# Optimization experiments

Measured on AMD Instinct MI355X. Metric: run time of the kernel, lower is better.

Reference implementation:

```python
import jax, jax.numpy as jnp
import numpy as np

V, C, TCTX, H, L = 32000, 768, 1024, 12, 6
B, T = 2, 1024
D = C // H
EPS = 1e-5


def setup_inputs() -> dict:
    key = jax.random.key(0)
    ks = jax.random.split(key, 12)
    s = lambda k, shape: jax.random.normal(k, shape, jnp.float32) * 0.02
    return {
        "x_indices": jax.random.randint(ks[0], (B, T), 0, V, jnp.int32),
        "tok_emb": s(ks[1], (V, C)),
        "pos_emb": s(ks[2], (TCTX, C)),
        "ln1_g": jnp.ones((L, C)), "ln1_b": jnp.zeros((L, C)),
        "wq": s(ks[3], (L, C, C)), "wk": s(ks[4], (L, C, C)), "wv": s(ks[5], (L, C, C)),
        "wo": s(ks[6], (L, C, C)), "bo": jnp.zeros((L, C)),
        "ln2_g": jnp.ones((L, C)), "ln2_b": jnp.zeros((L, C)),
        "w1": s(ks[7], (L, C, 4 * C)), "b1": jnp.zeros((L, 4 * C)),
        "w2": s(ks[8], (L, 4 * C, C)), "b2": jnp.zeros((L, C)),
        "lnf_g": jnp.ones((C,)), "lnf_b": jnp.zeros((C,)),
        "wp": s(ks[9], (C, V)), "bp": jnp.zeros((V,)),
    }


def _ln(x, g, b):
    m = x.mean(-1, keepdims=True)
    v = ((x - m) ** 2).mean(-1, keepdims=True)
    return (x - m) * jax.lax.rsqrt(v + EPS) * g + b


def _forward(x_indices, tok_emb, pos_emb, ln1_g, ln1_b, wq, wk, wv, wo, bo,
             ln2_g, ln2_b, w1, b1, w2, b2, lnf_g, lnf_b, wp, bp):
    Bv, Tv = x_indices.shape
    x = tok_emb[x_indices] + pos_emb[:Tv]  # [B,T,C]
    mask = jnp.tril(jnp.ones((Tv, Tv), dtype=bool))  # causal

    def block(x, p):
        g1, be1, q_w, k_w, v_w, o_w, o_b, g2, be2, f1, fb1, f2, fb2 = p
        h = _ln(x, g1, be1)
        q = (h @ q_w).reshape(Bv, Tv, H, D)
        k = (h @ k_w).reshape(Bv, Tv, H, D)
        v = (h @ v_w).reshape(Bv, Tv, H, D)
        scores = jnp.einsum('bthd,bshd->bhts', q, k) / jnp.sqrt(jnp.float32(D))
        scores = jnp.where(mask, scores, -jnp.inf)
        a = jax.nn.softmax(scores, axis=-1)
        o = jnp.einsum('bhts,bshd->bthd', a, v).reshape(Bv, Tv, C)
        x = x + o @ o_w + o_b
        h2 = _ln(x, g2, be2)
        x = x + jax.nn.relu(h2 @ f1 + fb1) @ f2 + fb2
        return x, None

    layer_params = (ln1_g, ln1_b, wq, wk, wv, wo, bo, ln2_g, ln2_b, w1, b1, w2, b2)
    x, _ = jax.lax.scan(block, x, layer_params)
    x = _ln(x, lnf_g, lnf_b)
    return x @ wp + bp  # logits [B,T,V]


def reference(x_indices, tok_emb, pos_emb, ln1_g, ln1_b, wq, wk, wv, wo, bo,
              ln2_g, ln2_b, w1, b1, w2, b2, lnf_g, lnf_b, wp, bp):
    return _forward(x_indices, tok_emb, pos_emb, ln1_g, ln1_b, wq, wk, wv, wo, bo,
                    ln2_g, ln2_b, w1, b1, w2, b2, lnf_g, lnf_b, wp, bp)
```

## Files before the change

### kernel.cpp

```cpp
#include <hip/hip_runtime.h>
#include <stdint.h>

#define DEV __device__ __forceinline__

typedef unsigned short u16;
typedef __attribute__((ext_vector_type(8))) short short8;
typedef __attribute__((ext_vector_type(4))) float floatx4;

#define B_ 2
#define T_ 1024
#define C_ 768
#define H_ 12
#define L_ 6
#define V_ 32000
#define F_ 3072
#define M_ 2048
#define C3_ 2304

#define VMW(n) asm volatile("s_waitcnt vmcnt(" #n ")" ::: "memory")
#define LGKM0 asm volatile("s_waitcnt lgkmcnt(0)" ::: "memory")
#define SBAR __builtin_amdgcn_s_barrier()
#define SCHED0 __builtin_amdgcn_sched_barrier(0)

DEV u16 f2bf(float f) {
  unsigned int u; __builtin_memcpy(&u, &f, 4);
  u += 0x7FFFu + ((u >> 16) & 1u);
  return (u16)(u >> 16);
}

DEV void gload16(const void* g, void* l) {
  __builtin_amdgcn_global_load_lds(
      (__attribute__((address_space(1))) void*)(uintptr_t)g,
      (__attribute__((address_space(3))) void*)(unsigned int)(uintptr_t)l,
      16, 0, 0);
}

DEV int xcd_swz(int flat, int nwg) {
  int q = nwg >> 3, r = nwg & 7;
  int xcd = flat & 7, sid = flat >> 3;
  return (xcd < r ? xcd * (q + 1) : r * (q + 1) + (xcd - r) * q) + sid;
}

__global__ __launch_bounds__(256) void transpose_f32_bf16(
    const float* __restrict__ src, u16* __restrict__ dst, int R, int Cc,
    size_t src_z, size_t dst_z) {
  __shared__ float tile[32][33];
  const float* s = src + (size_t)blockIdx.z * src_z;
  u16* d = dst + (size_t)blockIdx.z * dst_z;
  int c0 = blockIdx.x * 32, r0 = blockIdx.y * 32;
  int tx = threadIdx.x & 31, ty = threadIdx.x >> 5;
#pragma unroll
  for (int i = 0; i < 4; i++)
    tile[ty + 8 * i][tx] = s[(size_t)(r0 + ty + 8 * i) * Cc + (c0 + tx)];
  __syncthreads();
#pragma unroll
  for (int i = 0; i < 4; i++)
    d[(size_t)(c0 + ty + 8 * i) * R + (r0 + tx)] = f2bf(tile[tx][ty + 8 * i]);
}

__global__ __launch_bounds__(256) void transpose4_qkvo(
    const float* __restrict__ wq, const float* __restrict__ wk,
    const float* __restrict__ wv, const float* __restrict__ wo,
    u16* __restrict__ wqkvT, u16* __restrict__ woT) {
  __shared__ float tile[32][33];
  int z = blockIdx.z;
  int l = z >> 2, wsel = z & 3;
  size_t CC = (size_t)C_ * C_;
  const float* s = (wsel == 0 ? wq : wsel == 1 ? wk : wsel == 2 ? wv : wo) + (size_t)l * CC;
  u16* d = (wsel < 3) ? (wqkvT + (size_t)l * 3 * CC + (size_t)wsel * CC)
                      : (woT + (size_t)l * CC);
  int c0 = blockIdx.x * 32, r0 = blockIdx.y * 32;
  int tx = threadIdx.x & 31, ty = threadIdx.x >> 5;
#pragma unroll
  for (int i = 0; i < 4; i++)
    tile[ty + 8 * i][tx] = s[(size_t)(r0 + ty + 8 * i) * C_ + (c0 + tx)];
  __syncthreads();
#pragma unroll
  for (int i = 0; i < 4; i++)
    d[(size_t)(c0 + ty + 8 * i) * C_ + (r0 + tx)] = f2bf(tile[tx][ty + 8 * i]);
}

__global__ __launch_bounds__(256) void embed_ln(
    const int* __restrict__ idx, const float* __restrict__ tok,
    const float* __restrict__ pos, const float* __restrict__ g,
    const float* __restrict__ b, float* __restrict__ x, u16* __restrict__ out) {
  int row = blockIdx.x;
  int t = row & (T_ - 1);
  int tk = idx[row];
  const float* tp = tok + (size_t)tk * C_;
  const float* pp = pos + (size_t)t * C_;
  float* xp = x + (size_t)row * C_;
  int tid = threadIdx.x;
  float v0 = tp[tid] + pp[tid];
  float v1 = tp[tid + 256] + pp[tid + 256];
  float v2 = tp[tid + 512] + pp[tid + 512];
  xp[tid] = v0; xp[tid + 256] = v1; xp[tid + 512] = v2;
  float s = v0 + v1 + v2;
  float ss = v0 * v0 + v1 * v1 + v2 * v2;
#pragma unroll
  for (int o = 32; o > 0; o >>= 1) { s += __shfl_down(s, o); ss += __shfl_down(ss, o); }
  __shared__ float red[8];
  int wid = tid >> 6;
  if ((tid & 63) == 0) { red[wid] = s; red[4 + wid] = ss; }
  __syncthreads();
  float tot = red[0] + red[1] + red[2] + red[3];
  float tss = red[4] + red[5] + red[6] + red[7];
  float mean = tot * (1.f / C_);
  float var = tss * (1.f / C_) - mean * mean;
  float rstd = rsqrtf(var + 1e-5f);
  u16* op = out + (size_t)row * C_;
  op[tid]       = f2bf((v0 - mean) * rstd * g[tid]       + b[tid]);
  op[tid + 256] = f2bf((v1 - mean) * rstd * g[tid + 256] + b[tid + 256]);
  op[tid + 512] = f2bf((v2 - mean) * rstd * g[tid + 512] + b[tid + 512]);
}

__global__ __launch_bounds__(256) void ln_kernel(
    const float* __restrict__ x, const float* __restrict__ g,
    const float* __restrict__ b, u16* __restrict__ out) {
  int row = blockIdx.x;
  int tid = threadIdx.x;
  const float* xp = x + (size_t)row * C_;
  float v0 = xp[tid], v1 = xp[tid + 256], v2 = xp[tid + 512];
  float s = v0 + v1 + v2;
  float ss = v0 * v0 + v1 * v1 + v2 * v2;
#pragma unroll
  for (int o = 32; o > 0; o >>= 1) { s += __shfl_down(s, o); ss += __shfl_down(ss, o); }
  __shared__ float red[8];
  int wid = tid >> 6;
  if ((tid & 63) == 0) { red[wid] = s; red[4 + wid] = ss; }
  __syncthreads();
  float tot = red[0] + red[1] + red[2] + red[3];
  float tss = red[4] + red[5] + red[6] + red[7];
  float mean = tot * (1.f / C_);
  float var = tss * (1.f / C_) - mean * mean;
  float rstd = rsqrtf(var + 1e-5f);
  u16* op = out + (size_t)row * C_;
  op[tid]       = f2bf((v0 - mean) * rstd * g[tid]       + b[tid]);
  op[tid + 256] = f2bf((v1 - mean) * rstd * g[tid + 256] + b[tid + 256]);
  op[tid + 512] = f2bf((v2 - mean) * rstd * g[tid + 512] + b[tid + 512]);
}

template <int THREADS, int BM, int BN, int WM, int WN, int BIAS, int RELU, int OUTMODE, int SPLITK>
__global__ __launch_bounds__(THREADS) void gemm3(
    const u16* __restrict__ A, const u16* __restrict__ BT,
    const float* __restrict__ bias,
    u16* __restrict__ ob, float* __restrict__ fout, u16* __restrict__ vt,
    int N, int K) {
  constexpr int ALOADS = (BM * 64) / (THREADS * 16);
  constexpr int BLOADS = (BN * 64) / (THREADS * 16);
  constexpr int LDS_L = ALOADS + BLOADS;
  constexpr int MF = BM / (WM * 16);
  constexpr int NF = BN / (WN * 16);
  __shared__ __align__(16) u16 As[3][BM * 32];
  __shared__ __align__(16) u16 Bs[3][BN * 32];

  int tid = threadIdx.x;
  int lane = tid & 63, w = tid >> 6;
  int wm = w / WN, wn = w % WN;
  int rr = lane & 15, qg = lane >> 4;

  int gx = gridDim.x;
  int nwg = gx * gridDim.y;
  int flat = blockIdx.y * gx + blockIdx.x;
  int wg = xcd_swz(flat, nwg);
  int m0 = (wg % gx) * BM, n0 = (wg / gx) * BN;

  int kz = SPLITK > 1 ? blockIdx.z : 0;
  int Keff = SPLITK > 1 ? (K / SPLITK) : K;
  int kbase = kz * Keff;

  const u16* Aps[ALOADS];
  const u16* Bps[BLOADS];
#pragma unroll
  for (int i = 0; i < ALOADS; i++) {
    int idx = i * THREADS + tid;
    int row = idx >> 2;
    int chunk = (idx & 3) ^ ((row >> 1) & 3);
    Aps[i] = A + (size_t)(m0 + row) * K + chunk * 8 + kbase;
  }
#pragma unroll
  for (int i = 0; i < BLOADS; i++) {
    int idx = i * THREADS + tid;
    int row = idx >> 2;
    int chunk = (idx & 3) ^ ((row >> 1) & 3);
    Bps[i] = BT + (size_t)(n0 + row) * K + chunk * 8 + kbase;
  }

  auto stage = [&](int sl, int kk) {
#pragma unroll
    for (int i = 0; i < ALOADS; i++)
      gload16(Aps[i] + kk, (char*)As + (size_t)sl * BM * 64 + i * THREADS * 16 + w * 1024);
#pragma unroll
    for (int i = 0; i < BLOADS; i++)
      gload16(Bps[i] + kk, (char*)Bs + (size_t)sl * BN * 64 + i * THREADS * 16 + w * 1024);
  };

  floatx4 zero = {0.f, 0.f, 0.f, 0.f};
  floatx4 acc[MF][NF];
#pragma unroll
  for (int i = 0; i < MF; i++)
#pragma unroll
    for (int j = 0; j < NF; j++) acc[i][j] = zero;

  int NT = Keff >> 5;
  stage(0, 0);
  stage(1, 32);
  if constexpr (LDS_L == 2) VMW(2);
  else if constexpr (LDS_L == 3) VMW(3);
  else if constexpr (LDS_L == 4) VMW(4);
  else VMW(6);
  SBAR;
  SCHED0;

  int sqA = (qg ^ ((rr >> 1) & 3)) << 4;

  for (int t = 0; t < NT; ++t) {
    int sl = t % 3;
    if (t + 2 < NT) stage((t + 2) % 3, (t + 2) << 5);
    SCHED0;
    const char* Ab = (const char*)As + (size_t)sl * BM * 64;
    const char* Bb = (const char*)Bs + (size_t)sl * BN * 64;
    short8 af[MF], bf[NF];
#pragma unroll
    for (int i = 0; i < MF; i++)
      af[i] = *(const short8*)(Ab + ((wm * (BM / WM) + i * 16 + rr) << 6) + sqA);
#pragma unroll
    for (int j = 0; j < NF; j++)
      bf[j] = *(const short8*)(Bb + ((wn * (BN / WN) + j * 16 + rr) << 6) + sqA);
    __builtin_amdgcn_s_setprio(1);
#pragma unroll
    for (int i = 0; i < MF; i++)
#pragma unroll
      for (int j = 0; j < NF; j++)
        acc[i][j] = __builtin_amdgcn_mfma_f32_16x16x32_bf16(af[i], bf[j], acc[i][j], 0, 0, 0);
    __builtin_amdgcn_s_setprio(0);
    if (t < NT - 2) {
      if constexpr (LDS_L == 2) VMW(2);
      else if constexpr (LDS_L == 3) VMW(3);
      else if constexpr (LDS_L == 4) VMW(4);
      else VMW(6);
    } else if (t == NT - 2) VMW(0);
    if (t < NT - 1) { SBAR; SCHED0; }
  }

  int cb = n0 + wn * (BN / WN);
  int rb = m0 + wm * (BM / WM);
  bool isv = (OUTMODE == 3) && (n0 >= 1536);
#pragma unroll
  for (int i = 0; i < MF; i++) {
#pragma unroll
    for (int j = 0; j < NF; j++) {
      int col = cb + j * 16 + rr;
      float bv = 0.f;
      if (BIAS && kz == 0) bv = bias[col];
      float vals[4];
#pragma unroll
      for (int r = 0; r < 4; r++) {
        float val = acc[i][j][r] + bv;
        if (RELU) val = fmaxf(val, 0.f);
        vals[r] = val;
      }
      int row0 = rb + i * 16 + qg * 4;
      if (isv) {
        int colv = col - 1536;
        int bb = row0 >> 10, t0 = row0 & (T_ - 1);
        uint2 pk;
        pk.x = (unsigned int)f2bf(vals[0]) | ((unsigned int)f2bf(vals[1]) << 16);
        pk.y = (unsigned int)f2bf(vals[2]) | ((unsigned int)f2bf(vals[3]) << 16);
        *(uint2*)&vt[((size_t)bb * C_ + colv) * T_ + t0] = pk;
      } else {
#pragma unroll
        for (int r = 0; r < 4; r++) {
          size_t o = (size_t)(row0 + r) * N + col;
          if (OUTMODE == 0 || OUTMODE == 3) ob[o] = f2bf(vals[r]);
          else if (OUTMODE == 1) {
            if (SPLITK > 1) atomicAdd(&fout[o], vals[r]);
            else fout[o] += vals[r];
          } else fout[o] = vals[r];
        }
      }
    }
  }
}

__global__ __launch_bounds__(512) void gemm8(
    const u16* __restrict__ A, const u16* __restrict__ BT,
    const float* __restrict__ bias, float* __restrict__ fout, int N, int K) {
  __shared__ __align__(16) u16 As[2][2][128 * 64];
  __shared__ __align__(16) u16 Bs[2][2][128 * 64];
  int tid = threadIdx.x;
  int lane = tid & 63, w = tid >> 6;
  int wr = w >> 2, wc = w & 3;
  int rr = lane & 15, qg = lane >> 4;

  int gx = gridDim.x;
  int nwg = gx * gridDim.y;
  int flat = blockIdx.y * gx + blockIdx.x;
  int wg = xcd_swz(flat, nwg);
  int m0 = (wg % gx) * 256, n0 = (wg / gx) * 256;

  int la = tid >> 3;
  int sa = (((tid & 7) ^ (la & 7)) << 3);
  const u16* Ap0 = A + (size_t)(m0 + la) * K + sa;
  const u16* Ap1 = A + (size_t)(m0 + 128 + la) * K + sa;
  int lb0 = la, lb1 = 64 + la;
  const u16* Bp0 = BT + (size_t)(n0 + (lb0 >> 5) * 64 + (lb0 & 31)) * K + sa;
  const u16* Bp1 = BT + (size_t)(n0 + (lb1 >> 5) * 64 + (lb1 & 31)) * K + sa;

  auto stA = [&](int buf, int mh, int kt) {
    size_t off = (size_t)mh * 64 * K + kt * 64;
    gload16(Ap0 + off, (char*)&As[buf][mh][0] + w * 1024);
    gload16(Ap1 + off, (char*)&As[buf][mh][0] + 8192 + w * 1024);
  };
  auto stB = [&](int buf, int nh, int kt) {
    size_t off = (size_t)nh * 32 * K + kt * 64;
    gload16(Bp0 + off, (char*)&Bs[buf][nh][0] + w * 1024);
    gload16(Bp1 + off, (char*)&Bs[buf][nh][0] + 8192 + w * 1024);
  };
  auto stageOrd = [&](int buf, int h, int kt) {
    if (h == 0) stA(buf, 0, kt);
    else if (h == 1) stB(buf, 0, kt);
    else if (h == 2) stB(buf, 1, kt);
    else stA(buf, 1, kt);
  };

  floatx4 zero = {0.f, 0.f, 0.f, 0.f};
  floatx4 acc[8][4];
#pragma unroll
  for (int i = 0; i < 8; i++)
#pragma unroll
    for (int j = 0; j < 4; j++) acc[i][j] = zero;

  short8 a[2][4], b[2][2];
  int NKT = K >> 6;
  int NIT = NKT >> 1;

  stageOrd(0, 0, 0); stageOrd(0, 1, 0); stageOrd(0, 2, 0); stageOrd(0, 3, 0);
  VMW(4);
  SBAR;
  SCHED0;

  for (int it = 0; it < NIT; ++it) {
    int kt2 = it * 2;
    bool last = (it == NIT - 1);
#pragma unroll
    for (int p = 0; p < 8; ++p) {
      const int d = p >> 2;
      const int q = p & 3;
      const int mh = q >> 1, nh = q & 1;
      const char* Abp = (const char*)&As[d][mh][0];
      const char* Bbp = (const char*)&Bs[d][nh][0];
      if (q == 0 || q == 2) {
#pragma unroll
        for (int kk = 0; kk < 2; kk++)
#pragma unroll
          for (int i = 0; i < 4; i++) {
            int l = wr * 64 + i * 16 + rr;
            a[kk][i] = *(const short8*)(Abp + l * 128 + ((((kk << 2) + qg) ^ (rr & 7)) << 4));
          }
      }
#pragma unroll
      for (int kk = 0; kk < 2; kk++)
#pragma unroll
        for (int j = 0; j < 2; j++) {
          int l = wc * 32 + j * 16 + rr;
          b[kk][j] = *(const short8*)(Bbp + l * 128 + ((((kk << 2) + qg) ^ (rr & 7)) << 4));
        }
      if (p < 4) stageOrd(1, q, kt2 + 1);
      else if (!last) stageOrd(0, q, kt2 + 2);
      SCHED0;
      SBAR;
      LGKM0;
      SCHED0;
      __builtin_amdgcn_s_setprio(1);
#pragma unroll
      for (int kk = 0; kk < 2; kk++)
#pragma unroll
        for (int i = 0; i < 4; i++)
#pragma unroll
          for (int j = 0; j < 2; j++)
            acc[mh * 4 + i][nh * 2 + j] = __builtin_amdgcn_mfma_f32_16x16x32_bf16(
                a[kk][i], b[kk][j], acc[mh * 4 + i][nh * 2 + j], 0, 0, 0);
      __builtin_amdgcn_s_setprio(0);
      if (!last || p < 4) VMW(4);
      else if (p == 4) VMW(2);
      else if (p == 5) VMW(0);
      SBAR;
      SCHED0;
    }
  }

  int rbase = m0 + wr * 128;
  int cbase = n0 + wc * 64;
#pragma unroll
  for (int fi = 0; fi < 8; fi++) {
    int row0 = rbase + (fi >> 2) * 64 + (fi & 3) * 16 + qg * 4;
#pragma unroll
    for (int fj = 0; fj < 4; fj++) {
      int col = cbase + (fj >> 1) * 32 + (fj & 1) * 16 + rr;
      float bv = bias[col];
#pragma unroll
      for (int r = 0; r < 4; r++)
        fout[(size_t)(row0 + r) * N + col] = acc[fi][fj][r] + bv;
    }
  }
}

__global__ __launch_bounds__(256) void attn_kernel(
    const u16* __restrict__ qkv, const u16* __restrict__ vt, u16* __restrict__ o) {
  __shared__ __align__(16) u16 P_s[4][16 * 48];
  __shared__ float mls[3][2][16];
  __shared__ float osm[3][16][64];
  int nwg = gridDim.x;
  int wg = xcd_swz(blockIdx.x, nwg);
  int qt = wg & 63;
  int h = (wg >> 6) % H_;
  int b = wg / (64 * H_);
  int q0 = qt << 4;
  int tid = threadIdx.x;
  int ws = tid >> 6;
  int lane = tid & 63;
  int rr = lane & 15, qg = lane >> 4, kq = qg << 3;

  const u16* qb = qkv + (size_t)(b * T_ + q0 + rr) * C3_ + h * 64;
  short8 qf0 = *(const short8*)(qb + kq);
  short8 qf1 = *(const short8*)(qb + 32 + kq);

  float m_r = -1e30f, l_r = 0.f;
  floatx4 zero = {0.f, 0.f, 0.f, 0.f};
  floatx4 oacc[4];
#pragma unroll
  for (int d = 0; d < 4; d++) oacc[d] = zero;

  const u16* kbase = qkv + (size_t)(b * T_) * C3_ + 768 + h * 64;
  const u16* vbase = vt + (size_t)(b * C_ + h * 64) * T_;

  for (int kt0 = ws * 32; kt0 <= q0 + 15; kt0 += 128) {
    floatx4 s[2];
#pragma unroll
    for (int c = 0; c < 2; c++) {
      const u16* kb = kbase + (size_t)(kt0 + c * 16 + rr) * C3_;
      short8 kf0 = *(const short8*)(kb + kq);
      short8 kf1 = *(const short8*)(kb + 32 + kq);
      floatx4 z = zero;
      z = __builtin_amdgcn_mfma_f32_16x16x32_bf16(kf0, qf0, z, 0, 0, 0);
      z = __builtin_amdgcn_mfma_f32_16x16x32_bf16(kf1, qf1, z, 0, 0, 0);
      s[c] = z;
    }
    int qpos = q0 + rr;
    float p[2][4];
    float mx = -1e30f;
#pragma unroll
    for (int c = 0; c < 2; c++)
#pragma unroll
      for (int r = 0; r < 4; r++) {
        int kpos = kt0 + c * 16 + qg * 4 + r;
        float val = s[c][r] * 0.125f;
        val = (kpos <= qpos) ? val : -1e30f;
        p[c][r] = val;
        mx = fmaxf(mx, val);
      }
    mx = fmaxf(mx, __shfl_xor(mx, 16));
    mx = fmaxf(mx, __shfl_xor(mx, 32));
    float mn = fmaxf(m_r, mx);
    float escL = exp2f((m_r - mn) * 1.44269504f);
    m_r = mn;
    float ps = 0.f;
#pragma unroll
    for (int c = 0; c < 2; c++)
#pragma unroll
      for (int r = 0; r < 4; r++) {
        float pv = exp2f((p[c][r] - mn) * 1.44269504f);
        p[c][r] = pv;
        ps += pv;
      }
    ps += __shfl_xor(ps, 16);
    ps += __shfl_xor(ps, 32);
    l_r = l_r * escL + ps;
#pragma unroll
    for (int c = 0; c < 2; c++) {
      unsigned int u0 = (unsigned int)f2bf(p[c][0]) | ((unsigned int)f2bf(p[c][1]) << 16);
      unsigned int u1 = (unsigned int)f2bf(p[c][2]) | ((unsigned int)f2bf(p[c][3]) << 16);
      uint2 pk; pk.x = u0; pk.y = u1;
      *(uint2*)&P_s[ws][rr * 48 + c * 16 + qg * 4] = pk;
    }
    float er[4];
#pragma unroll
    for (int r = 0; r < 4; r++) er[r] = __shfl(escL, qg * 4 + r);
#pragma unroll
    for (int d = 0; d < 4; d++)
#pragma unroll
      for (int r = 0; r < 4; r++) oacc[d][r] *= er[r];
    short8 pa = *(const short8*)&P_s[ws][rr * 48 + kq];
#pragma unroll
    for (int d = 0; d < 4; d++) {
      short8 vf = *(const short8*)(vbase + (size_t)(d * 16 + rr) * T_ + kt0 + kq);
      oacc[d] = __builtin_amdgcn_mfma_f32_16x16x32_bf16(pa, vf, oacc[d], 0, 0, 0);
    }
  }

  if (ws != 0) {
    if (qg == 0) { mls[ws - 1][0][rr] = m_r; mls[ws - 1][1][rr] = l_r; }
#pragma unroll
    for (int d = 0; d < 4; d++)
#pragma unroll
      for (int r = 0; r < 4; r++)
        osm[ws - 1][qg * 4 + r][d * 16 + rr] = oacc[d][r];
  }
  __syncthreads();
  if (ws == 0) {
#pragma unroll
    for (int s2 = 0; s2 < 3; s2++) {
      float mw = mls[s2][0][rr];
      float lw = mls[s2][1][rr];
      float mn = fmaxf(m_r, mw);
      float e0 = exp2f((m_r - mn) * 1.44269504f);
      float e1 = exp2f((mw - mn) * 1.44269504f);
      m_r = mn;
      l_r = l_r * e0 + lw * e1;
      float er0[4], er1[4];
#pragma unroll
      for (int r = 0; r < 4; r++) {
        er0[r] = __shfl(e0, qg * 4 + r);
        er1[r] = __shfl(e1, qg * 4 + r);
      }
#pragma unroll
      for (int d = 0; d < 4; d++)
#pragma unroll
        for (int r = 0; r < 4; r++)
          oacc[d][r] = oacc[d][r] * er0[r] + osm[s2][qg * 4 + r][d * 16 + rr] * er1[r];
    }
    float lb[4];
#pragma unroll
    for (int r = 0; r < 4; r++) lb[r] = __shfl(l_r, qg * 4 + r);
    u16* obp = o + (size_t)(b * T_ + q0) * C_ + h * 64;
#pragma unroll
    for (int d = 0; d < 4; d++)
#pragma unroll
      for (int r = 0; r < 4; r++) {
        int row = qg * 4 + r;
        obp[(size_t)row * C_ + d * 16 + rr] = f2bf(oacc[d][r] / lb[r]);
      }
  }
}

extern "C" void kernel_launch(void* const* d_in, const int* in_sizes, int n_in,
                              void* d_out, int out_size, void* d_ws, size_t ws_size,
                              hipStream_t stream) {
  (void)in_sizes; (void)n_in; (void)out_size; (void)ws_size;
  const int*   xidx = (const int*)d_in[0];
  const float* tok  = (const float*)d_in[1];
  const float* pos  = (const float*)d_in[2];
  const float* ln1g = (const float*)d_in[3];
  const float* ln1b = (const float*)d_in[4];
  const float* wq   = (const float*)d_in[5];
  const float* wk   = (const float*)d_in[6];
  const float* wv   = (const float*)d_in[7];
  const float* wo   = (const float*)d_in[8];
  const float* bo   = (const float*)d_in[9];
  const float* ln2g = (const float*)d_in[10];
  const float* ln2b = (const float*)d_in[11];
  const float* w1   = (const float*)d_in[12];
  const float* b1   = (const float*)d_in[13];
  const float* w2   = (const float*)d_in[14];
  const float* b2   = (const float*)d_in[15];
  const float* lnfg = (const float*)d_in[16];
  const float* lnfb = (const float*)d_in[17];
  const float* wp   = (const float*)d_in[18];
  const float* bp   = (const float*)d_in[19];

  char* ws = (char*)d_ws;
  size_t off = 0;
  auto alloc = [&](size_t bytes) { char* p = ws + off; off += (bytes + 255) & ~(size_t)255; return p; };
  u16* wqkvT = (u16*)alloc((size_t)L_ * 3 * C_ * C_ * 2);
  u16* woT = (u16*)alloc((size_t)L_ * C_ * C_ * 2);
  u16* w1T = (u16*)alloc((size_t)L_ * C_ * F_ * 2);
  u16* w2T = (u16*)alloc((size_t)L_ * C_ * F_ * 2);
  u16* wpT = (u16*)alloc((size_t)C_ * V_ * 2);
  float* x = (float*)alloc((size_t)M_ * C_ * 4);
  u16* hb   = (u16*)alloc((size_t)M_ * C_ * 2);
  u16* qkvb = (u16*)alloc((size_t)M_ * C3_ * 2);
  u16* vtb  = (u16*)alloc((size_t)M_ * C_ * 2);
  u16* aob  = (u16*)alloc((size_t)M_ * C_ * 2);
  u16* mb   = (u16*)alloc((size_t)M_ * F_ * 2);

  dim3 blk(256);
  size_t CC = (size_t)C_ * C_, CF = (size_t)C_ * F_;
  transpose4_qkvo<<<dim3(C_ / 32, C_ / 32, L_ * 4), blk, 0, stream>>>(
      wq, wk, wv, wo, wqkvT, woT);
  transpose_f32_bf16<<<dim3(F_ / 32, C_ / 32, L_), blk, 0, stream>>>(w1, w1T, C_, F_, CF, CF);
  transpose_f32_bf16<<<dim3(C_ / 32, F_ / 32, L_), blk, 0, stream>>>(w2, w2T, F_, C_, CF, CF);
  transpose_f32_bf16<<<dim3(V_ / 32, C_ / 32, 1), blk, 0, stream>>>(wp, wpT, C_, V_, 0, 0);
  embed_ln<<<M_, blk, 0, stream>>>(xidx, tok, pos, ln1g, ln1b, x, hb);

  for (int l = 0; l < L_; ++l) {
    size_t wOff = (size_t)l * 3 * CC;
    size_t oOff = (size_t)l * CC;
    size_t fOff = (size_t)l * CF;
    if (l > 0)
      ln_kernel<<<M_, blk, 0, stream>>>(x, ln1g + l * C_, ln1b + l * C_, hb);
    gemm3<256, 128, 128, 2, 2, 0, 0, 3, 1><<<dim3(M_ / 128, C3_ / 128), 256, 0, stream>>>(
        hb, wqkvT + wOff, nullptr, qkvb, nullptr, vtb, C3_, C_);
    attn_kernel<<<B_ * H_ * (T_ / 16), dim3(256), 0, stream>>>(qkvb, vtb, aob);
    gemm3<256, 128, 128, 2, 2, 1, 0, 1, 2><<<dim3(M_ / 128, C_ / 128, 2), 256, 0, stream>>>(
        aob, woT + oOff, bo + l * C_, nullptr, x, nullptr, C_, C_);
    ln_kernel<<<M_, blk, 0, stream>>>(x, ln2g + l * C_, ln2b + l * C_, hb);
    gemm3<256, 128, 128, 2, 2, 1, 1, 0, 1><<<dim3(M_ / 128, F_ / 128), 256, 0, stream>>>(
        hb, w1T + fOff, b1 + l * F_, mb, nullptr, nullptr, F_, C_);
    gemm3<256, 128, 128, 2, 2, 1, 0, 1, 2><<<dim3(M_ / 128, C_ / 128, 2), 256, 0, stream>>>(
        mb, w2T + fOff, b2 + l * C_, nullptr, x, nullptr, C_, F_);
  }
  ln_kernel<<<M_, blk, 0, stream>>>(x, lnfg, lnfb, hb);
  gemm8<<<dim3(M_ / 256, V_ / 256), 512, 0, stream>>>(
      hb, wpT, bp, (float*)d_out, V_, C_);
}
```

Measured before the change: 1.026 ms.

## Replace split-K atomic residual adds with partial buffers summed in LayerNorm

The Wo and W2 split-K GEMMs now write their two K-partials to separate fp32 buffers with plain stores instead of atomicAdd into the residual. A new ln_sum kernel adds both partials to the residual, writes the updated residual back, and applies the following LayerNorm. This removes atomic read-modify-write traffic and keeps the LN launch count unchanged. In exchange it adds an extra 12 MB partial buffer and additional fp32 reads in the LN kernel.

```diff
diff --git a/kernel.cpp b/kernel.cpp
--- a/kernel.cpp
+++ b/kernel.cpp
@@ -114,13 +114,19 @@
   op[tid + 512] = f2bf((v2 - mean) * rstd * g[tid + 512] + b[tid + 512]);
 }
 
-__global__ __launch_bounds__(256) void ln_kernel(
-    const float* __restrict__ x, const float* __restrict__ g,
-    const float* __restrict__ b, u16* __restrict__ out) {
+__global__ __launch_bounds__(256) void ln_sum(
+    float* __restrict__ x, const float* __restrict__ p0, const float* __restrict__ p1,
+    const float* __restrict__ g, const float* __restrict__ b, u16* __restrict__ out) {
   int row = blockIdx.x;
   int tid = threadIdx.x;
-  const float* xp = x + (size_t)row * C_;
-  float v0 = xp[tid], v1 = xp[tid + 256], v2 = xp[tid + 512];
+  size_t base = (size_t)row * C_;
+  float* xp = x + base;
+  const float* q0 = p0 + base;
+  const float* q1 = p1 + base;
+  float v0 = xp[tid]       + q0[tid]       + q1[tid];
+  float v1 = xp[tid + 256] + q0[tid + 256] + q1[tid + 256];
+  float v2 = xp[tid + 512] + q0[tid + 512] + q1[tid + 512];
+  xp[tid] = v0; xp[tid + 256] = v1; xp[tid + 512] = v2;
   float s = v0 + v1 + v2;
   float ss = v0 * v0 + v1 * v1 + v2 * v2;
 #pragma unroll
@@ -246,6 +252,8 @@
   int cb = n0 + wn * (BN / WN);
   int rb = m0 + wm * (BM / WM);
   bool isv = (OUTMODE == 3) && (n0 >= 1536);
+  float* fo = fout;
+  if (OUTMODE == 4) fo = fout + (size_t)kz * M_ * N;
 #pragma unroll
   for (int i = 0; i < MF; i++) {
 #pragma unroll
@@ -273,10 +281,7 @@
         for (int r = 0; r < 4; r++) {
           size_t o = (size_t)(row0 + r) * N + col;
           if (OUTMODE == 0 || OUTMODE == 3) ob[o] = f2bf(vals[r]);
-          else if (OUTMODE == 1) {
-            if (SPLITK > 1) atomicAdd(&fout[o], vals[r]);
-            else fout[o] += vals[r];
-          } else fout[o] = vals[r];
+          else fo[o] = vals[r];
         }
       }
     }
@@ -578,11 +583,13 @@
   u16* w2T = (u16*)alloc((size_t)L_ * C_ * F_ * 2);
   u16* wpT = (u16*)alloc((size_t)C_ * V_ * 2);
   float* x = (float*)alloc((size_t)M_ * C_ * 4);
+  float* ps0 = (float*)alloc((size_t)2 * M_ * C_ * 4);
   u16* hb   = (u16*)alloc((size_t)M_ * C_ * 2);
   u16* qkvb = (u16*)alloc((size_t)M_ * C3_ * 2);
   u16* vtb  = (u16*)alloc((size_t)M_ * C_ * 2);
   u16* aob  = (u16*)alloc((size_t)M_ * C_ * 2);
   u16* mb   = (u16*)alloc((size_t)M_ * F_ * 2);
+  float* ps1 = ps0 + (size_t)M_ * C_;
 
   dim3 blk(256);
   size_t CC = (size_t)C_ * C_, CF = (size_t)C_ * F_;
@@ -597,20 +604,20 @@
     size_t wOff = (size_t)l * 3 * CC;
     size_t oOff = (size_t)l * CC;
     size_t fOff = (size_t)l * CF;
-    if (l > 0)
-      ln_kernel<<<M_, blk, 0, stream>>>(x, ln1g + l * C_, ln1b + l * C_, hb);
     gemm3<256, 128, 128, 2, 2, 0, 0, 3, 1><<<dim3(M_ / 128, C3_ / 128), 256, 0, stream>>>(
         hb, wqkvT + wOff, nullptr, qkvb, nullptr, vtb, C3_, C_);
     attn_kernel<<<B_ * H_ * (T_ / 16), dim3(256), 0, stream>>>(qkvb, vtb, aob);
-    gemm3<256, 128, 128, 2, 2, 1, 0, 1, 2><<<dim3(M_ / 128, C_ / 128, 2), 256, 0, stream>>>(
-        aob, woT + oOff, bo + l * C_, nullptr, x, nullptr, C_, C_);
-    ln_kernel<<<M_, blk, 0, stream>>>(x, ln2g + l * C_, ln2b + l * C_, hb);
+    gemm3<256, 128, 128, 2, 2, 1, 0, 4, 2><<<dim3(M_ / 128, C_ / 128, 2), 256, 0, stream>>>(
+        aob, woT + oOff, bo + l * C_, nullptr, ps0, nullptr, C_, C_);
+    ln_sum<<<M_, blk, 0, stream>>>(x, ps0, ps1, ln2g + l * C_, ln2b + l * C_, hb);
     gemm3<256, 128, 128, 2, 2, 1, 1, 0, 1><<<dim3(M_ / 128, F_ / 128), 256, 0, stream>>>(
         hb, w1T + fOff, b1 + l * F_, mb, nullptr, nullptr, F_, C_);
-    gemm3<256, 128, 128, 2, 2, 1, 0, 1, 2><<<dim3(M_ / 128, C_ / 128, 2), 256, 0, stream>>>(
-        mb, w2T + fOff, b2 + l * C_, nullptr, x, nullptr, C_, F_);
-  }
-  ln_kernel<<<M_, blk, 0, stream>>>(x, lnfg, lnfb, hb);
+    gemm3<256, 128, 128, 2, 2, 1, 0, 4, 2><<<dim3(M_ / 128, C_ / 128, 2), 256, 0, stream>>>(
+        mb, w2T + fOff, b2 + l * C_, nullptr, ps0, nullptr, C_, F_);
+    if (l + 1 < L_)
+      ln_sum<<<M_, blk, 0, stream>>>(x, ps0, ps1, ln1g + (l + 1) * C_, ln1b + (l + 1) * C_, hb);
+  }
+  ln_sum<<<M_, blk, 0, stream>>>(x, ps0, ps1, lnfg, lnfb, hb);
   gemm8<<<dim3(M_ / 256, V_ / 256), 512, 0, stream>>>(
       hb, wpT, bp, (float*)d_out, V_, C_);
 }
```

Result: faster. 1.004 ms (-2.1%).
